# Performance work log

Hardware: AMD Instinct MI355X
Metric: run time of the kernel (lower is better)

The kernel has to match this reference:

```python
import jax, jax.numpy as jnp
import numpy as np

B, K, C = 512, 64, 2048  # batch, mixture components, copy (eval points)


def setup_inputs() -> dict:
    key = jax.random.key(0)
    kw, km, ks, kr, kx = jax.random.split(key, 5)
    w = jax.random.uniform(kw, (B, K), dtype=jnp.float32)            # mixture weights
    means = jax.random.normal(km, (B, K, 2), dtype=jnp.float32)      # mean1, mean2
    sds = jax.random.uniform(ks, (B, K, 2), dtype=jnp.float32,
                             minval=0.5, maxval=1.5)                 # sd1, sd2 (>0)
    corr = jax.random.uniform(kr, (B, K), dtype=jnp.float32,
                              minval=-0.8, maxval=0.8)               # |corr| < 1
    model_out = jnp.concatenate(
        [w[..., None], means, sds, corr[..., None]], axis=-1)        # [B, K, 6]
    X = jax.random.normal(kx, (B, C, 2), dtype=jnp.float32)
    return {"model_out": model_out, "X": X}


def reference(model_out, X):
    # Unpack params: w, mean1, mean2, sd1, sd2, corr  -- each [B, K]
    w = model_out[..., 0]
    m1 = model_out[..., 1]
    m2 = model_out[..., 2]
    s1 = model_out[..., 3]
    s2 = model_out[..., 4]
    r = model_out[..., 5]

    # Closed-form bivariate normal pdf (equivalent to Cholesky-based
    # MultivariateNormal log_prob for the 2x2 covariance built in torch).
    # dx, dy: [B, C, K] via broadcasting X[B,C,1] against params[B,1,K]
    dx = (X[:, :, 0:1] - m1[:, None, :]) / s1[:, None, :]
    dy = (X[:, :, 1:2] - m2[:, None, :]) / s2[:, None, :]
    rb = r[:, None, :]
    omr2 = 1.0 - rb * rb  # 1 - rho^2
    z = dx * dx - 2.0 * rb * dx * dy + dy * dy
    two_pi = 2.0 * jnp.pi
    norm = two_pi * s1[:, None, :] * s2[:, None, :] * jnp.sqrt(omr2)
    probs = jnp.exp(-0.5 * z / omr2) / norm  # [B, C, K]

    # Weighted sum over components -> [B, C]
    return jnp.einsum('bck,bk->bc', probs, w)
```

## Files before the change

kernel.cpp:

```cpp
#include <hip/hip_runtime.h>


typedef float v2f __attribute__((ext_vector_type(2)));

constexpr int B = 512;
constexpr int K = 64;
constexpr int C = 2048;
constexpr int BLOCK = 256;
constexpr int HALVES = 2;
constexpr int CH = C / HALVES;

__global__ __launch_bounds__(BLOCK, 4) void mixture_kernel(
    const float* __restrict__ mo,
    const float* __restrict__ X,
    float* __restrict__ out)
{
    __shared__ float4 P[K][2];

    const int bid = blockIdx.x;
    const int b   = bid >> 1;
    const int h   = bid & 1;
    const int t   = threadIdx.x;

    if (t < K) {
        const float* p6 = mo + ((size_t)(b * K + t)) * 6;
        const float w  = p6[0];
        const float m1 = p6[1];
        const float m2 = p6[2];
        const float s1 = p6[3];
        const float s2 = p6[4];
        const float r  = p6[5];

        const float omr2 = fmaf(-r, r, 1.0f);
        const float inv  = 1.0f / omr2;
        const float g    = 0.7213475204444817f * inv;
        const float i1   = 1.0f / s1;
        const float i2   = 1.0f / s2;
        const float p    = g * i1 * i1;
        const float q    = g * i2 * i2;
        const float s    = 2.0f * r * g * i1 * i2;
        const float A    = -p;
        const float Bc   = -q;
        const float Cc   = s;
        const float D    = fmaf(2.0f * p, m1, -s * m2);
        const float E    = fmaf(2.0f * q, m2, -s * m1);
        const float wn   = w * 0.15915494309189535f * i1 * i2 * sqrtf(inv);
        const float L    = log2f(fmaxf(wn, 1e-37f));
        const float F    = fmaf(-p, m1 * m1, fmaf(-q, m2 * m2, fmaf(s, m1 * m2, L)));

        P[t][0] = make_float4(A, Bc, Cc, D);
        P[t][1] = make_float4(E, F, 0.0f, 0.0f);
    }
    __syncthreads();

    const float4* Xb = (const float4*)(X + ((size_t)b * C + (size_t)h * CH) * 2);
    const float4 xv0 = Xb[t];
    const float4 xv1 = Xb[t + BLOCK];

    const v2f xp[2] = { {xv0.x, xv0.z}, {xv1.x, xv1.z} };
    const v2f yp[2] = { {xv0.y, xv0.w}, {xv1.y, xv1.w} };
    v2f acc[2] = { {0.0f, 0.0f}, {0.0f, 0.0f} };

#pragma unroll 4
    for (int k = 0; k < K; ++k) {
        const float4 c0 = P[k][0];
        const float4 c1 = P[k][1];
        const v2f cAB = { c0.x, c0.y };
        const v2f cCD = { c0.z, c0.w };
        const v2f cEF = { c1.x, c1.y };

#pragma unroll
        for (int j = 0; j < 2; ++j) {
            v2f u, vv, e;
            asm("v_pk_fma_f32 %0, %1, %2, %1 op_sel:[0,0,1] op_sel_hi:[0,1,1]"
                : "=v"(u) : "v"(cCD), "v"(yp[j]));
            asm("v_pk_fma_f32 %0, %1, %2, %0 op_sel:[0,0,0] op_sel_hi:[0,1,1]"
                : "+v"(u) : "v"(cAB), "v"(xp[j]));
            asm("v_pk_fma_f32 %0, %1, %2, %3 op_sel:[1,0,0] op_sel_hi:[1,1,0]"
                : "=v"(vv) : "v"(cAB), "v"(yp[j]), "v"(cEF));
            asm("v_pk_fma_f32 %0, %1, %2, %3 op_sel:[0,0,1] op_sel_hi:[1,1,1]"
                : "=v"(e) : "v"(yp[j]), "v"(vv), "v"(cEF));
            e = __builtin_elementwise_fma(xp[j], u, e);
            v2f ex;
            ex.x = __builtin_amdgcn_exp2f(e.x);
            ex.y = __builtin_amdgcn_exp2f(e.y);
            acc[j] = acc[j] + ex;
        }
    }

    float2* ob = (float2*)(out + (size_t)b * C + (size_t)h * CH);
    ob[t]         = make_float2(acc[0].x, acc[0].y);
    ob[t + BLOCK] = make_float2(acc[1].x, acc[1].y);
}

extern "C" void kernel_launch(void* const* d_in, const int* in_sizes, int n_in,
                              void* d_out, int out_size, void* d_ws, size_t ws_size,
                              hipStream_t stream) {
    const float* mo = (const float*)d_in[0];
    const float* X  = (const float*)d_in[1];
    float* out      = (float*)d_out;

    mixture_kernel<<<dim3(B * HALVES), dim3(BLOCK), 0, stream>>>(mo, X, out);
}
```

Measured before the change: 70.76 us.

## Precompute coefficients in separate kernel and read them as scalar SGPR operands

Moves the per-component coefficient computation into a separate small kernel that writes to workspace, and the main kernel reads coefficients through uniform 64-bit loads so they land in scalar registers used directly as packed-FMA operands. This drops the LDS staging and the barrier. The work is also split into quarters with one point-pair per thread and a higher occupancy hint. The cost is an extra kernel launch, a global round trip for the coefficients, and less ILP per thread.

```diff
diff --git a/kernel.cpp b/kernel.cpp
--- a/kernel.cpp
+++ b/kernel.cpp
@@ -2,95 +2,91 @@
 
 
 typedef float v2f __attribute__((ext_vector_type(2)));
+typedef unsigned long long u64;
 
 constexpr int B = 512;
 constexpr int K = 64;
 constexpr int C = 2048;
 constexpr int BLOCK = 256;
-constexpr int HALVES = 2;
-constexpr int CH = C / HALVES;
+constexpr int QUARTERS = 4;
+constexpr int CQ = C / QUARTERS;
 
-__global__ __launch_bounds__(BLOCK, 4) void mixture_kernel(
+__global__ __launch_bounds__(BLOCK) void coef_kernel(
     const float* __restrict__ mo,
+    float* __restrict__ coef)
+{
+    const int i = blockIdx.x * BLOCK + threadIdx.x;
+    const float* p6 = mo + (size_t)i * 6;
+    const float w  = p6[0];
+    const float m1 = p6[1];
+    const float m2 = p6[2];
+    const float s1 = p6[3];
+    const float s2 = p6[4];
+    const float r  = p6[5];
+
+    const float omr2 = fmaf(-r, r, 1.0f);
+    const float inv  = 1.0f / omr2;
+    const float g    = 0.7213475204444817f * inv;
+    const float i1   = 1.0f / s1;
+    const float i2   = 1.0f / s2;
+    const float p    = g * i1 * i1;
+    const float q    = g * i2 * i2;
+    const float s    = 2.0f * r * g * i1 * i2;
+    const float A    = -p;
+    const float Bc   = -q;
+    const float Cc   = s;
+    const float D    = fmaf(2.0f * p, m1, -s * m2);
+    const float E    = fmaf(2.0f * q, m2, -s * m1);
+    const float wn   = w * 0.15915494309189535f * i1 * i2 * sqrtf(inv);
+    const float L    = log2f(fmaxf(wn, 1e-37f));
+    const float F    = fmaf(-p, m1 * m1, fmaf(-q, m2 * m2, fmaf(s, m1 * m2, L)));
+
+    float4* cp = (float4*)(coef + (size_t)i * 8);
+    cp[0] = make_float4(Cc, D, Bc, E);
+    cp[1] = make_float4(A, F, 0.0f, 0.0f);
+}
+
+__global__ __launch_bounds__(BLOCK, 8) void mixture_main(
+    const float* __restrict__ coef,
     const float* __restrict__ X,
     float* __restrict__ out)
 {
-    __shared__ float4 P[K][2];
-
     const int bid = blockIdx.x;
-    const int b   = bid >> 1;
-    const int h   = bid & 1;
+    const int b   = bid >> 2;
+    const int q   = bid & 3;
     const int t   = threadIdx.x;
 
-    if (t < K) {
-        const float* p6 = mo + ((size_t)(b * K + t)) * 6;
-        const float w  = p6[0];
-        const float m1 = p6[1];
-        const float m2 = p6[2];
-        const float s1 = p6[3];
-        const float s2 = p6[4];
-        const float r  = p6[5];
+    const float4 xv = ((const float4*)(X + ((size_t)b * C + (size_t)q * CQ) * 2))[t];
+    const v2f xp = { xv.x, xv.z };
+    const v2f yp = { xv.y, xv.w };
+    v2f acc = { 0.0f, 0.0f };
 
-        const float omr2 = fmaf(-r, r, 1.0f);
-        const float inv  = 1.0f / omr2;
-        const float g    = 0.7213475204444817f * inv;
-        const float i1   = 1.0f / s1;
-        const float i2   = 1.0f / s2;
-        const float p    = g * i1 * i1;
-        const float q    = g * i2 * i2;
-        const float s    = 2.0f * r * g * i1 * i2;
-        const float A    = -p;
-        const float Bc   = -q;
-        const float Cc   = s;
-        const float D    = fmaf(2.0f * p, m1, -s * m2);
-        const float E    = fmaf(2.0f * q, m2, -s * m1);
-        const float wn   = w * 0.15915494309189535f * i1 * i2 * sqrtf(inv);
-        const float L    = log2f(fmaxf(wn, 1e-37f));
-        const float F    = fmaf(-p, m1 * m1, fmaf(-q, m2 * m2, fmaf(s, m1 * m2, L)));
-
-        P[t][0] = make_float4(A, Bc, Cc, D);
-        P[t][1] = make_float4(E, F, 0.0f, 0.0f);
-    }
-    __syncthreads();
-
-    const float4* Xb = (const float4*)(X + ((size_t)b * C + (size_t)h * CH) * 2);
-    const float4 xv0 = Xb[t];
-    const float4 xv1 = Xb[t + BLOCK];
-
-    const v2f xp[2] = { {xv0.x, xv0.z}, {xv1.x, xv1.z} };
-    const v2f yp[2] = { {xv0.y, xv0.w}, {xv1.y, xv1.w} };
-    v2f acc[2] = { {0.0f, 0.0f}, {0.0f, 0.0f} };
+    const u64* cb = (const u64*)coef + (size_t)b * (K * 4);
 
 #pragma unroll 4
     for (int k = 0; k < K; ++k) {
-        const float4 c0 = P[k][0];
-        const float4 c1 = P[k][1];
-        const v2f cAB = { c0.x, c0.y };
-        const v2f cCD = { c0.z, c0.w };
-        const v2f cEF = { c1.x, c1.y };
+        const u64 pCD = cb[4 * k + 0];
+        const u64 pBE = cb[4 * k + 1];
+        const u64 pAF = cb[4 * k + 2];
 
-#pragma unroll
-        for (int j = 0; j < 2; ++j) {
-            v2f u, vv, e;
-            asm("v_pk_fma_f32 %0, %1, %2, %1 op_sel:[0,0,1] op_sel_hi:[0,1,1]"
-                : "=v"(u) : "v"(cCD), "v"(yp[j]));
-            asm("v_pk_fma_f32 %0, %1, %2, %0 op_sel:[0,0,0] op_sel_hi:[0,1,1]"
-                : "+v"(u) : "v"(cAB), "v"(xp[j]));
-            asm("v_pk_fma_f32 %0, %1, %2, %3 op_sel:[1,0,0] op_sel_hi:[1,1,0]"
-                : "=v"(vv) : "v"(cAB), "v"(yp[j]), "v"(cEF));
-            asm("v_pk_fma_f32 %0, %1, %2, %3 op_sel:[0,0,1] op_sel_hi:[1,1,1]"
-                : "=v"(e) : "v"(yp[j]), "v"(vv), "v"(cEF));
-            e = __builtin_elementwise_fma(xp[j], u, e);
-            v2f ex;
-            ex.x = __builtin_amdgcn_exp2f(e.x);
-            ex.y = __builtin_amdgcn_exp2f(e.y);
-            acc[j] = acc[j] + ex;
-        }
+        v2f u, vv, e;
+        asm("v_pk_fma_f32 %0, %1, %2, %1 op_sel:[0,0,1] op_sel_hi:[0,1,1]"
+            : "=v"(u) : "s"(pCD), "v"(yp));
+        asm("v_pk_fma_f32 %0, %1, %2, %0 op_sel:[0,0,0] op_sel_hi:[0,1,1]"
+            : "+v"(u) : "s"(pAF), "v"(xp));
+        asm("v_pk_fma_f32 %0, %1, %2, %1 op_sel:[0,0,1] op_sel_hi:[0,1,1]"
+            : "=v"(vv) : "s"(pBE), "v"(yp));
+        asm("v_pk_fma_f32 %0, %1, %2, %3 op_sel:[0,0,1] op_sel_hi:[1,1,1]"
+            : "=v"(e) : "v"(yp), "v"(vv), "s"(pAF));
+        e = __builtin_elementwise_fma(xp, u, e);
+
+        v2f ex;
+        ex.x = __builtin_amdgcn_exp2f(e.x);
+        ex.y = __builtin_amdgcn_exp2f(e.y);
+        acc = acc + ex;
     }
 
-    float2* ob = (float2*)(out + (size_t)b * C + (size_t)h * CH);
-    ob[t]         = make_float2(acc[0].x, acc[0].y);
-    ob[t + BLOCK] = make_float2(acc[1].x, acc[1].y);
+    ((float2*)(out + (size_t)b * C + (size_t)q * CQ))[t] = make_float2(acc.x, acc.y);
 }
 
 extern "C" void kernel_launch(void* const* d_in, const int* in_sizes, int n_in,
@@ -99,6 +95,8 @@
     const float* mo = (const float*)d_in[0];
     const float* X  = (const float*)d_in[1];
     float* out      = (float*)d_out;
+    float* coef     = (float*)d_ws;
 
-    mixture_kernel<<<dim3(B * HALVES), dim3(BLOCK), 0, stream>>>(mo, X, out);
+    coef_kernel<<<dim3(B * K / BLOCK), dim3(BLOCK), 0, stream>>>(mo, coef);
+    mixture_main<<<dim3(B * QUARTERS), dim3(BLOCK), 0, stream>>>(coef, X, out);
 }
```

Result: slower. 76.94 us (+8.7%).
